# Optimization experiments

Measured on AMD Instinct MI355X. Metric: run time of the kernel, lower is better.

## Reference

```python
import jax, jax.numpy as jnp
import numpy as np

B, T, H = 4, 2048, 512
HEADS = 8
D = H // HEADS  # head dim = 64


def setup_inputs() -> dict:
    key = jax.random.key(0)
    ks = jax.random.split(key, 5)
    s = 1.0 / np.sqrt(H)
    return {
        "x": jax.random.normal(ks[0], (B, T, H), dtype=jnp.float32),
        "w_qkv": jax.random.uniform(ks[1], (H, 3 * H), dtype=jnp.float32, minval=-s, maxval=s),
        "b_qkv": jax.random.uniform(ks[2], (3 * H,), dtype=jnp.float32, minval=-s, maxval=s),
        "w_proj": jax.random.uniform(ks[3], (H, H), dtype=jnp.float32, minval=-s, maxval=s),
        "b_proj": jax.random.uniform(ks[4], (H,), dtype=jnp.float32, minval=-s, maxval=s),
    }


def reference(x, w_qkv, b_qkv, w_proj, b_proj):
    b, t, h = x.shape
    scale = (h // HEADS) ** (-0.5)
    qkv = (x @ w_qkv + b_qkv).reshape(b, t, 3, HEADS, h // HEADS)
    q, k, v = qkv[:, :, 0], qkv[:, :, 1], qkv[:, :, 2]  # [b,t,heads,d]
    q = q * scale
    scores = jnp.einsum('bthd,bThd->bhtT', q, k)  # [b,heads,t,t]
    weights = jax.nn.softmax(scores, axis=-1)
    attn = jnp.einsum('bhtT,bThd->bthd', weights, v).reshape(b, t, h)
    return attn @ w_proj + b_proj
```

## Files before the change

### kernel.cpp

```cpp
#include <hip/hip_runtime.h>
#include <stdint.h>

typedef unsigned short u16;
typedef __attribute__((ext_vector_type(8))) __bf16 bf16x8;
typedef __attribute__((ext_vector_type(4))) __bf16 bf16x4;
typedef __attribute__((ext_vector_type(4))) float f32x4;
typedef __attribute__((ext_vector_type(2))) unsigned int u32x2;
typedef __attribute__((ext_vector_type(4))) unsigned int u32x4;

#define QSCALE 0.18033688011112042f

__device__ __forceinline__ u16 f2bf(float f) {
    uint32_t u = __builtin_bit_cast(uint32_t, f);
    u = (u + 0x7fffu + ((u >> 16) & 1u)) >> 16;
    return (u16)u;
}
__device__ __forceinline__ float bf2f(u16 h) {
    uint32_t u = ((uint32_t)h) << 16;
    return __builtin_bit_cast(float, u);
}

__device__ __forceinline__ void gl_lds16(const u16* g, u16* l) {
    __builtin_amdgcn_global_load_lds(
        (__attribute__((address_space(1))) uint32_t*)(g),
        (__attribute__((address_space(3))) uint32_t*)(l), 16, 0, 0);
}

__global__ __launch_bounds__(256) void convert_x_k(const float* __restrict__ xf,
                                                   u16* __restrict__ xbf) {
    const size_t v = (size_t)blockIdx.x * 256 + threadIdx.x;
    const f32x4 val = ((const f32x4*)xf)[v];
    u32x2 p;
    p.x = (uint32_t)f2bf(val.x) | ((uint32_t)f2bf(val.y) << 16);
    p.y = (uint32_t)f2bf(val.z) | ((uint32_t)f2bf(val.w) << 16);
    *(u32x2*)&xbf[v * 4] = p;
}

__global__ void transpose_cvt_k(const float* __restrict__ in,
                                u16* __restrict__ out, int R, int C) {
    __shared__ u16 t[64][65];
    const int bx = blockIdx.x << 6, by = blockIdx.y << 6;
    const int tx = threadIdx.x, ty = threadIdx.y;
#pragma unroll
    for (int i = ty; i < 64; i += 8)
        t[i][tx] = f2bf(in[(size_t)(by + i) * C + bx + tx]);
    __syncthreads();
#pragma unroll
    for (int i = ty; i < 64; i += 8) out[(size_t)(bx + i) * R + by + tx] = t[tx][i];
}

template <int EPI>
__global__ __launch_bounds__(256) void gemm_bt_k(
    const u16* __restrict__ A, const u16* __restrict__ Bt,
    const float* __restrict__ bias,
    u16* __restrict__ Qb, u16* __restrict__ Kb, u16* __restrict__ Vt,
    float* __restrict__ OutF) {
    __shared__ u16 lA[2][128 * 32];
    __shared__ u16 lB[2][128 * 32];
    const int tid = threadIdx.x;
    const int w = tid >> 6, l = tid & 63, quad = l >> 4, r = l & 15;
    const int tm = blockIdx.x << 7, tn = blockIdx.y << 7;
    const int wm = (w >> 1) << 6, wn = (w & 1) << 6;
    const int srow = l >> 2, sch = (l & 3) << 3;

    f32x4 acc[4][4];
#pragma unroll
    for (int i = 0; i < 4; ++i)
#pragma unroll
        for (int j = 0; j < 4; ++j) acc[i][j] = (f32x4){0.f, 0.f, 0.f, 0.f};

    auto stage = [&](int b, int kk) {
#pragma unroll
        for (int ii = 0; ii < 2; ++ii) {
            const int rowl = w * 32 + ii * 16;
            gl_lds16(A + (size_t)(tm + rowl + srow) * 512 + kk + sch, &lA[b][rowl * 32]);
            gl_lds16(Bt + (size_t)(tn + rowl + srow) * 512 + kk + sch, &lB[b][rowl * 32]);
        }
    };

    stage(0, 0);
    __syncthreads();

    int cur = 0;
    for (int kk = 0; kk < 512; kk += 32) {
        if (kk + 32 < 512) stage(cur ^ 1, kk + 32);
        bf16x8 af[4], bfr[4];
#pragma unroll
        for (int mi = 0; mi < 4; ++mi)
            af[mi] = *(const bf16x8*)&lA[cur][(wm + mi * 16 + r) * 32 + quad * 8];
#pragma unroll
        for (int ni = 0; ni < 4; ++ni)
            bfr[ni] = *(const bf16x8*)&lB[cur][(wn + ni * 16 + r) * 32 + quad * 8];
#pragma unroll
        for (int mi = 0; mi < 4; ++mi)
#pragma unroll
            for (int ni = 0; ni < 4; ++ni)
                acc[mi][ni] = __builtin_amdgcn_mfma_f32_16x16x32_bf16(
                    af[mi], bfr[ni], acc[mi][ni], 0, 0, 0);
        __syncthreads();
        cur ^= 1;
    }

#pragma unroll
    for (int ni = 0; ni < 4; ++ni) {
        const int n = tn + wn + ni * 16 + r;
        const float bv = bias[n];
        const int which = n >> 9, head = (n >> 6) & 7, d = n & 63;
#pragma unroll
        for (int mi = 0; mi < 4; ++mi) {
#pragma unroll
            for (int i = 0; i < 4; ++i) {
                const int m = tm + wm + mi * 16 + quad * 4 + i;
                const float v = acc[mi][ni][i] + bv;
                if (EPI == 0) {
                    const int bb = m >> 11, t = m & 2047;
                    const int bh = bb * 8 + head;
                    if (which == 0)
                        Qb[((size_t)(bh * 2048 + t) << 6) + d] = f2bf(v * QSCALE);
                    else if (which == 1)
                        Kb[((size_t)(bh * 2048 + t) << 6) + d] = f2bf(v);
                    else
                        Vt[((size_t)(bh * 64 + d) << 11) + t] = f2bf(v);
                } else {
                    OutF[(size_t)m * 512 + n] = v;
                }
            }
        }
    }
}

__global__ __launch_bounds__(256, 2) void attn_k(
    const u16* __restrict__ Qb, const u16* __restrict__ Kb,
    const u16* __restrict__ Vt, u16* __restrict__ attnb) {
    __shared__ u16 lk[2][64 * 64];
    __shared__ u16 lv[2][64 * 64];
    const int tid = threadIdx.x;
    const int w = tid >> 6, l = tid & 63, quad = l >> 4, r = l & 15;
    const int qt = blockIdx.x, bh = blockIdx.y;
    const size_t qbase = (size_t)bh * 2048 + qt * 128;
    const int srl = l >> 3;
    const int sg = (l & 7) ^ srl;

    const int rl = r & 7;
    const int rhi = r >> 3;
    const int skq = (r & 3) ^ (((r >> 2) & 1) << 1) ^ (((r >> 2) & 2) << 1);
    const int g0 = (quad ^ skq) << 3;

    bf16x8 qf[2][2];
#pragma unroll
    for (int qs = 0; qs < 2; ++qs)
#pragma unroll
        for (int hf = 0; hf < 2; ++hf)
            qf[qs][hf] = *(const bf16x8*)&Qb[((qbase + w * 32 + qs * 16 + r) << 6) +
                                            hf * 32 + quad * 8];

    const u32x4 onesu = {0x3F803F80u, 0x3F803F80u, 0x3F803F80u, 0x3F803F80u};
    const bf16x8 vones = __builtin_bit_cast(bf16x8, onesu);

    f32x4 o[2][4];
#pragma unroll
    for (int qs = 0; qs < 2; ++qs)
#pragma unroll
        for (int i = 0; i < 4; ++i) o[qs][i] = (f32x4){0.f, 0.f, 0.f, 0.f};
    f32x4 osum[2];
    osum[0] = (f32x4){0.f, 0.f, 0.f, 0.f};
    osum[1] = (f32x4){0.f, 0.f, 0.f, 0.f};

    auto stage = [&](int b, int kv0) {
#pragma unroll
        for (int ii = 0; ii < 2; ++ii) {
            const int chunk = w * 2 + ii;
            const int skr = (srl & 3) ^ ((chunk & 1) << 1) ^ ((chunk & 2) << 1);
            gl_lds16(Kb + ((size_t)(bh * 2048 + kv0 + chunk * 8 + srl) << 6) +
                         ((l & 7) ^ skr) * 8,
                     &lk[b][chunk * 512]);
            gl_lds16(Vt + (((size_t)(bh * 64 + chunk * 8 + srl)) << 11) + kv0 + sg * 8,
                     &lv[b][chunk * 512]);
        }
    };

    stage(0, 0);
    __syncthreads();

    int cur = 0;
    for (int kv0 = 0; kv0 < 2048; kv0 += 64) {
        if (kv0 + 64 < 2048) stage(cur ^ 1, kv0 + 64);

        bf16x8 ka[4], kb[4];
#pragma unroll
        for (int kt = 0; kt < 4; ++kt) {
            const int R = (kt & 1) * 32 + (r >> 2) * 8 + (kt >> 1) * 4 + (r & 3);
            ka[kt] = *(const bf16x8*)&lk[cur][R * 64 + g0];
            kb[kt] = *(const bf16x8*)&lk[cur][(R * 64 + g0) ^ 32];
        }
        bf16x8 vb[2][4];
#pragma unroll
        for (int h = 0; h < 2; ++h)
#pragma unroll
            for (int dt = 0; dt < 4; ++dt) {
                const int baseV = (dt * 2 + rhi) * 512 + rl * 64;
                vb[h][dt] = *(const bf16x8*)&lv[cur][baseV + ((h * 4 + quad) ^ rl) * 8];
            }

        bf16x4 pk4[2][4];
#pragma unroll
        for (int kt = 0; kt < 4; ++kt) {
#pragma unroll
            for (int qs = 0; qs < 2; ++qs) {
                f32x4 z = (f32x4){0.f, 0.f, 0.f, 0.f};
                __builtin_amdgcn_s_setprio(1);
                z = __builtin_amdgcn_mfma_f32_16x16x32_bf16(ka[kt], qf[qs][0], z, 0, 0, 0);
                z = __builtin_amdgcn_mfma_f32_16x16x32_bf16(kb[kt], qf[qs][1], z, 0, 0, 0);
                __builtin_amdgcn_s_setprio(0);
                bf16x4 pb;
                pb[0] = (__bf16)__builtin_amdgcn_exp2f(z[0]);
                pb[1] = (__bf16)__builtin_amdgcn_exp2f(z[1]);
                pb[2] = (__bf16)__builtin_amdgcn_exp2f(z[2]);
                pb[3] = (__bf16)__builtin_amdgcn_exp2f(z[3]);
                pk4[qs][kt] = pb;
            }
        }

        __builtin_amdgcn_s_setprio(1);
#pragma unroll
        for (int h = 0; h < 2; ++h) {
            const bf16x8 ap0 = __builtin_shufflevector(pk4[0][h], pk4[0][h + 2],
                                                       0, 1, 2, 3, 4, 5, 6, 7);
            const bf16x8 ap1 = __builtin_shufflevector(pk4[1][h], pk4[1][h + 2],
                                                       0, 1, 2, 3, 4, 5, 6, 7);
#pragma unroll
            for (int dt = 0; dt < 4; ++dt) {
                o[0][dt] = __builtin_amdgcn_mfma_f32_16x16x32_bf16(ap0, vb[h][dt],
                                                                  o[0][dt], 0, 0, 0);
                o[1][dt] = __builtin_amdgcn_mfma_f32_16x16x32_bf16(ap1, vb[h][dt],
                                                                  o[1][dt], 0, 0, 0);
            }
            osum[0] = __builtin_amdgcn_mfma_f32_16x16x32_bf16(ap0, vones, osum[0], 0, 0, 0);
            osum[1] = __builtin_amdgcn_mfma_f32_16x16x32_bf16(ap1, vones, osum[1], 0, 0, 0);
        }
        __builtin_amdgcn_s_setprio(0);

        __syncthreads();
        cur ^= 1;
    }

    const int bb = bh >> 3, head = bh & 7;
#pragma unroll
    for (int qs = 0; qs < 2; ++qs) {
#pragma unroll
        for (int i = 0; i < 4; ++i) {
            const float inv = __builtin_amdgcn_rcpf(osum[qs][i]);
            const int row = bb * 2048 + qt * 128 + w * 32 + qs * 16 + quad * 4 + i;
#pragma unroll
            for (int dt = 0; dt < 4; ++dt)
                attnb[(size_t)row * 512 + head * 64 + dt * 16 + r] =
                    f2bf(o[qs][dt][i] * inv);
        }
    }
}

extern "C" void kernel_launch(void* const* d_in, const int* in_sizes, int n_in,
                              void* d_out, int out_size, void* d_ws, size_t ws_size,
                              hipStream_t stream) {
    const float *x = nullptr, *wq = nullptr, *bq = nullptr, *wp = nullptr, *bp = nullptr;
    for (int i = 0; i < n_in; ++i) {
        switch (in_sizes[i]) {
            case 4194304: x  = (const float*)d_in[i]; break;
            case 786432:  wq = (const float*)d_in[i]; break;
            case 1536:    bq = (const float*)d_in[i]; break;
            case 262144:  wp = (const float*)d_in[i]; break;
            case 512:     bp = (const float*)d_in[i]; break;
        }
    }
    if (!x || !wq || !bq || !wp || !bp) {
        x = (const float*)d_in[0]; wq = (const float*)d_in[1];
        bq = (const float*)d_in[2]; wp = (const float*)d_in[3];
        bp = (const float*)d_in[4];
    }
    float* out = (float*)d_out;

    char* ws = (char*)d_ws;
    u16* attnb  = (u16*)(ws + 0);
    u16* wqkvT  = (u16*)(ws + 0);
    u16* Qb     = (u16*)(ws + 8388608);
    u16* wprojT = (u16*)(ws + 8388608);
    u16* Kb     = (u16*)(ws + 16777216);
    u16* Vt     = (u16*)(ws + 25165824);
    u16* xbf    = (u16*)d_out;

    convert_x_k<<<dim3(4096), 256, 0, stream>>>(x, xbf);
    transpose_cvt_k<<<dim3(24, 8), dim3(64, 8), 0, stream>>>(wq, wqkvT, 512, 1536);
    gemm_bt_k<0><<<dim3(64, 12), 256, 0, stream>>>(xbf, wqkvT, bq, Qb, Kb, Vt, nullptr);
    attn_k<<<dim3(16, 32), 256, 0, stream>>>(Qb, Kb, Vt, attnb);
    transpose_cvt_k<<<dim3(8, 8), dim3(64, 8), 0, stream>>>(wp, wprojT, 512, 512);
    gemm_bt_k<1><<<dim3(64, 4), 256, 0, stream>>>(attnb, wprojT, bp, nullptr, nullptr,
                                                  nullptr, out);
}
```

Baseline: 163.8 us.

## Fuse weight transpose-convert into GEMM loads and stage QKV epilogue through LDS

Removes the two transpose_cvt kernel launches by having the GEMM read fp32 weights directly, convert them to bf16 in registers, and write them transposed into LDS during the pipelined k-loop. The QKV epilogue now stages results in shared memory so Q/K/V (including the transposed V) are written with 16-byte coalesced stores instead of scattered 2-byte stores. The projection GEMM uses a narrower 64-column tile to launch more blocks, and launch bounds request 3 blocks per CU. The trade-off is extra fp32 weight traffic per block, since each block re-reads and re-converts its weights, plus scalar LDS writes for the B tile.

```diff
diff --git a/kernel.cpp b/kernel.cpp
--- a/kernel.cpp
+++ b/kernel.cpp
@@ -14,10 +14,6 @@
     uint32_t u = __builtin_bit_cast(uint32_t, f);
     u = (u + 0x7fffu + ((u >> 16) & 1u)) >> 16;
     return (u16)u;
-}
-__device__ __forceinline__ float bf2f(u16 h) {
-    uint32_t u = ((uint32_t)h) << 16;
-    return __builtin_bit_cast(float, u);
 }
 
 __device__ __forceinline__ void gl_lds16(const u16* g, u16* l) {
@@ -36,94 +32,150 @@
     *(u32x2*)&xbf[v * 4] = p;
 }
 
-__global__ void transpose_cvt_k(const float* __restrict__ in,
-                                u16* __restrict__ out, int R, int C) {
-    __shared__ u16 t[64][65];
-    const int bx = blockIdx.x << 6, by = blockIdx.y << 6;
-    const int tx = threadIdx.x, ty = threadIdx.y;
-#pragma unroll
-    for (int i = ty; i < 64; i += 8)
-        t[i][tx] = f2bf(in[(size_t)(by + i) * C + bx + tx]);
-    __syncthreads();
-#pragma unroll
-    for (int i = ty; i < 64; i += 8) out[(size_t)(bx + i) * R + by + tx] = t[tx][i];
-}
-
-template <int EPI>
-__global__ __launch_bounds__(256) void gemm_bt_k(
-    const u16* __restrict__ A, const u16* __restrict__ Bt,
+template <int EPI, int BN>
+__global__ __launch_bounds__(256, 3) void gemm_bt_k(
+    const u16* __restrict__ A, const float* __restrict__ Bw,
     const float* __restrict__ bias,
     u16* __restrict__ Qb, u16* __restrict__ Kb, u16* __restrict__ Vt,
     float* __restrict__ OutF) {
-    __shared__ u16 lA[2][128 * 32];
-    __shared__ u16 lB[2][128 * 32];
+    constexpr int MI = (BN == 128) ? 4 : 2;
+    constexpr int BC = (BN == 128) ? 1536 : 512;
+    constexpr int NB = BN * 32 / 256;
+    constexpr int SSTG = 2 * 128 * 32 + 2 * BN * 32;
+    constexpr int SMEM = (EPI == 0) ? (128 * 136 > SSTG ? 128 * 136 : SSTG) : SSTG;
+    __shared__ u16 smem[SMEM];
+    u16* lA = smem;
+    u16* lB = smem + 2 * 128 * 32;
+
     const int tid = threadIdx.x;
     const int w = tid >> 6, l = tid & 63, quad = l >> 4, r = l & 15;
-    const int tm = blockIdx.x << 7, tn = blockIdx.y << 7;
-    const int wm = (w >> 1) << 6, wn = (w & 1) << 6;
+    const int tm = blockIdx.x << 7;
+    const int tn = blockIdx.y * BN;
+    const int wm = (BN == 128) ? ((w >> 1) << 6) : (w << 5);
+    const int wn = (BN == 128) ? ((w & 1) << 6) : 0;
     const int srow = l >> 2, sch = (l & 3) << 3;
-
-    f32x4 acc[4][4];
-#pragma unroll
-    for (int i = 0; i < 4; ++i)
+    const int kc = tid & 31, ng = tid >> 5;
+
+    f32x4 acc[MI][4];
+#pragma unroll
+    for (int i = 0; i < MI; ++i)
 #pragma unroll
         for (int j = 0; j < 4; ++j) acc[i][j] = (f32x4){0.f, 0.f, 0.f, 0.f};
 
-    auto stage = [&](int b, int kk) {
+    auto stageA = [&](int b, int kk) {
 #pragma unroll
         for (int ii = 0; ii < 2; ++ii) {
             const int rowl = w * 32 + ii * 16;
-            gl_lds16(A + (size_t)(tm + rowl + srow) * 512 + kk + sch, &lA[b][rowl * 32]);
-            gl_lds16(Bt + (size_t)(tn + rowl + srow) * 512 + kk + sch, &lB[b][rowl * 32]);
+            gl_lds16(A + (size_t)(tm + rowl + srow) * 512 + kk + sch,
+                     &lA[b * 4096 + rowl * 32]);
         }
     };
 
-    stage(0, 0);
+    stageA(0, 0);
+    {
+        const float* bsrc = Bw + (size_t)kc * BC + tn + ng * NB;
+        f32x4 br[NB / 4];
+#pragma unroll
+        for (int j = 0; j < NB / 4; ++j) br[j] = ((const f32x4*)bsrc)[j];
+#pragma unroll
+        for (int e = 0; e < NB; ++e)
+            lB[(ng * NB + e) * 32 + kc] = f2bf(br[e / 4][e & 3]);
+    }
     __syncthreads();
 
     int cur = 0;
     for (int kk = 0; kk < 512; kk += 32) {
-        if (kk + 32 < 512) stage(cur ^ 1, kk + 32);
-        bf16x8 af[4], bfr[4];
-#pragma unroll
-        for (int mi = 0; mi < 4; ++mi)
-            af[mi] = *(const bf16x8*)&lA[cur][(wm + mi * 16 + r) * 32 + quad * 8];
+        const bool hn = (kk + 32) < 512;
+        f32x4 br[NB / 4];
+        if (hn) {
+            stageA(cur ^ 1, kk + 32);
+            const float* bsrc = Bw + (size_t)(kk + 32 + kc) * BC + tn + ng * NB;
+#pragma unroll
+            for (int j = 0; j < NB / 4; ++j) br[j] = ((const f32x4*)bsrc)[j];
+        }
+        bf16x8 af[MI], bfr[4];
+#pragma unroll
+        for (int mi = 0; mi < MI; ++mi)
+            af[mi] = *(const bf16x8*)&lA[cur * 4096 + (wm + mi * 16 + r) * 32 + quad * 8];
 #pragma unroll
         for (int ni = 0; ni < 4; ++ni)
-            bfr[ni] = *(const bf16x8*)&lB[cur][(wn + ni * 16 + r) * 32 + quad * 8];
-#pragma unroll
-        for (int mi = 0; mi < 4; ++mi)
+            bfr[ni] =
+                *(const bf16x8*)&lB[cur * BN * 32 + (wn + ni * 16 + r) * 32 + quad * 8];
+#pragma unroll
+        for (int mi = 0; mi < MI; ++mi)
 #pragma unroll
             for (int ni = 0; ni < 4; ++ni)
                 acc[mi][ni] = __builtin_amdgcn_mfma_f32_16x16x32_bf16(
                     af[mi], bfr[ni], acc[mi][ni], 0, 0, 0);
+        if (hn) {
+            u16* dB = &lB[(cur ^ 1) * BN * 32];
+#pragma unroll
+            for (int e = 0; e < NB; ++e)
+                dB[(ng * NB + e) * 32 + kc] = f2bf(br[e / 4][e & 3]);
+        }
         __syncthreads();
         cur ^= 1;
     }
 
-#pragma unroll
-    for (int ni = 0; ni < 4; ++ni) {
-        const int n = tn + wn + ni * 16 + r;
-        const float bv = bias[n];
-        const int which = n >> 9, head = (n >> 6) & 7, d = n & 63;
-#pragma unroll
-        for (int mi = 0; mi < 4; ++mi) {
-#pragma unroll
-            for (int i = 0; i < 4; ++i) {
-                const int m = tm + wm + mi * 16 + quad * 4 + i;
-                const float v = acc[mi][ni][i] + bv;
-                if (EPI == 0) {
-                    const int bb = m >> 11, t = m & 2047;
-                    const int bh = bb * 8 + head;
-                    if (which == 0)
-                        Qb[((size_t)(bh * 2048 + t) << 6) + d] = f2bf(v * QSCALE);
-                    else if (which == 1)
-                        Kb[((size_t)(bh * 2048 + t) << 6) + d] = f2bf(v);
+    if (EPI == 1) {
+#pragma unroll
+        for (int ni = 0; ni < 4; ++ni) {
+            const int n = tn + wn + ni * 16 + r;
+            const float bv = bias[n];
+#pragma unroll
+            for (int mi = 0; mi < MI; ++mi)
+#pragma unroll
+                for (int i = 0; i < 4; ++i) {
+                    const int m = tm + wm + mi * 16 + quad * 4 + i;
+                    OutF[(size_t)m * 512 + n] = acc[mi][ni][i] + bv;
+                }
+        }
+    } else {
+        const bool isV = (tn >= 1024);
+        const bool isQ = (tn < 512);
+#pragma unroll
+        for (int ni = 0; ni < 4; ++ni) {
+            const int nl = wn + ni * 16 + r;
+            const float bv = bias[tn + nl];
+#pragma unroll
+            for (int mi = 0; mi < MI; ++mi)
+#pragma unroll
+                for (int i = 0; i < 4; ++i) {
+                    const int ml = wm + mi * 16 + quad * 4 + i;
+                    float v = acc[mi][ni][i] + bv;
+                    if (isQ) v *= QSCALE;
+                    const u16 hb = f2bf(v);
+                    if (isV)
+                        smem[nl * 136 + ml] = hb;
                     else
-                        Vt[((size_t)(bh * 64 + d) << 11) + t] = f2bf(v);
-                } else {
-                    OutF[(size_t)m * 512 + n] = v;
+                        smem[ml * 136 + nl] = hb;
                 }
+        }
+        __syncthreads();
+        const int tbb = tm >> 11, tt = tm & 2047;
+        if (!isV) {
+            u16* base = isQ ? Qb : Kb;
+            const int mlr = l >> 3, ls = l & 7;
+#pragma unroll
+            for (int rg = 0; rg < 4; ++rg)
+#pragma unroll
+                for (int h = 0; h < 2; ++h) {
+                    const int ml = (w * 4 + rg) * 8 + mlr;
+                    const int head = ((tn + h * 64) >> 6) & 7;
+                    const int bh = tbb * 8 + head;
+                    const u32x4 dv = *(const u32x4*)&smem[ml * 136 + h * 64 + ls * 8];
+                    *(u32x4*)&base[((size_t)(bh * 2048 + tt + ml) << 6) + ls * 8] = dv;
+                }
+        } else {
+            const int nlr = l >> 4, ls = l & 15;
+#pragma unroll
+            for (int j2 = 0; j2 < 8; ++j2) {
+                const int nl = w * 32 + j2 * 4 + nlr;
+                const int n = tn + nl;
+                const int d = n & 63, head = (n >> 6) & 7;
+                const int bh = tbb * 8 + head;
+                const u32x4 dv = *(const u32x4*)&smem[nl * 136 + ls * 8];
+                *(u32x4*)&Vt[((size_t)(bh * 64 + d) << 11) + tt + ls * 8] = dv;
             }
         }
     }
@@ -281,18 +333,15 @@
 
     char* ws = (char*)d_ws;
     u16* attnb  = (u16*)(ws + 0);
-    u16* wqkvT  = (u16*)(ws + 0);
     u16* Qb     = (u16*)(ws + 8388608);
-    u16* wprojT = (u16*)(ws + 8388608);
     u16* Kb     = (u16*)(ws + 16777216);
     u16* Vt     = (u16*)(ws + 25165824);
     u16* xbf    = (u16*)d_out;
 
     convert_x_k<<<dim3(4096), 256, 0, stream>>>(x, xbf);
-    transpose_cvt_k<<<dim3(24, 8), dim3(64, 8), 0, stream>>>(wq, wqkvT, 512, 1536);
-    gemm_bt_k<0><<<dim3(64, 12), 256, 0, stream>>>(xbf, wqkvT, bq, Qb, Kb, Vt, nullptr);
+    gemm_bt_k<0, 128><<<dim3(64, 12), 256, 0, stream>>>(xbf, wq, bq, Qb, Kb, Vt,
+                                                        nullptr);
     attn_k<<<dim3(16, 32), 256, 0, stream>>>(Qb, Kb, Vt, attnb);
-    transpose_cvt_k<<<dim3(8, 8), dim3(64, 8), 0, stream>>>(wp, wprojT, 512, 512);
-    gemm_bt_k<1><<<dim3(64, 4), 256, 0, stream>>>(attnb, wprojT, bp, nullptr, nullptr,
-                                                  nullptr, out);
-}
+    gemm_bt_k<1, 64><<<dim3(64, 8), 256, 0, stream>>>(attnb, wp, bp, nullptr, nullptr,
+                                                      nullptr, out);
+}
```

Measured after the change: 170.9 us. +4.3%, slower.
